# Optimization experiments

Hardware: AMD Instinct MI355X
Metric: run time of the kernel (lower is better)

The kernel has to match this reference:

```python
import jax, jax.numpy as jnp
import jax.lax as lax
import numpy as np

G = 128    # number of asset groups (batch)
A = 100    # n_assets per group
WIN = 10   # window_size
FD = 16    # feature_dim
H = 128    # hidden_dim


def setup_inputs() -> dict:
    key = jax.random.key(0)
    ks = jax.random.split(key, 12)
    N = G * A
    def glorot(k, shape, fan_in):
        return (jax.random.normal(k, shape, jnp.float32) / np.sqrt(fan_in)).astype(jnp.float32)
    return {
        "x": jax.random.normal(ks[0], (N, WIN, FD), jnp.float32),
        "W1": glorot(ks[1], (WIN * FD, H), WIN * FD),
        "b1": jnp.zeros((H,), jnp.float32),
        "W2": glorot(ks[2], (H, H), H),
        "b2": jnp.zeros((H,), jnp.float32),
        "W3": glorot(ks[3], (H, H), H),
        "b3": jnp.zeros((H,), jnp.float32),
        "cw1": glorot(ks[4], (H, 1, 1, 3), 3),      # conv2d_1 weight [out,in,kh,kw]
        "cb1": jnp.zeros((H,), jnp.float32),
        "cw2": glorot(ks[5], (1, H, 1, 3), 3 * H),  # conv2d_2 weight
        "cb2": jnp.zeros((1,), jnp.float32),
    }


def _corrcoef(r):
    xc = r - r.mean(axis=1, keepdims=True)
    cov = xc @ xc.T                      # divisor cancels in correlation
    d = jnp.sqrt(jnp.diag(cov))
    return cov / (d[:, None] * d[None, :])


def _conv1x3(h, w, b):
    # h: [1,C,N,H]; kernel (1,3), padding (0,1) -> NCHW conv
    out = lax.conv_general_dilated(h, w, (1, 1), ((0, 0), (1, 1)),
                                   dimension_numbers=("NCHW", "OIHW", "NCHW"))
    return out + b[None, :, None, None]


def reference(x, W1, b1, W2, b2, W3, b3, cw1, cb1, cw2, cb2):
    # block-diagonal adjacency == independent per-group adjacencies
    returns = x[:, :, -1].reshape(G, A, WIN)
    corr = jax.vmap(_corrcoef)(returns)                  # [G,A,A]
    adj = 1.0 - jnp.abs(corr) + jnp.eye(A, dtype=x.dtype)
    dinv = 1.0 / jnp.sqrt(adj.sum(axis=-1))              # [G,A]
    norm_adj = dinv[:, :, None] * adj * dinv[:, None, :] # D^-1/2 A D^-1/2

    feats = x.reshape(G, A, WIN * FD)
    h = jax.nn.relu(jnp.einsum("gij,gjf->gif", norm_adj, feats) @ W1 + b1)
    h = jax.nn.relu(jnp.einsum("gij,gjh->gih", norm_adj, h) @ W2 + b2)
    h = jax.nn.relu(jnp.einsum("gij,gjh->gih", norm_adj, h) @ W3 + b3)

    h = h.reshape(1, 1, G * A, H)                        # [1,1,N,H]
    h = jax.nn.relu(_conv1x3(h, cw1, cb1))               # [1,H,N,H]
    out = _conv1x3(h, cw2, cb2)                          # [1,1,N,H]
    return out[0, 0]                                     # [N,H]
```

## Files before the change

kernel.cpp:

```cpp
#include <hip/hip_runtime.h>

#define G   128
#define A   100
#define WIN 10
#define FD  16
#define H   128
#define NROWS (G*A)
#define K1  (WIN*FD)

#define SST 136
#define YST 136
#define AST 40
#define H3ST 132

typedef __attribute__((ext_vector_type(8))) short short8;
typedef __attribute__((ext_vector_type(4))) short short4v;
typedef __attribute__((ext_vector_type(4))) float floatx4;
typedef __attribute__((ext_vector_type(2))) float pf2;

struct BfPair { short h, l; };

__device__ inline unsigned short f2bf(float f) {
    unsigned u = __float_as_uint(f);
    u += 0x7fff + ((u >> 16) & 1);
    return (unsigned short)(u >> 16);
}
__device__ inline float bf2f(unsigned short h) {
    return __uint_as_float(((unsigned)h) << 16);
}
__device__ inline BfPair split1(float v) {
    BfPair p;
    unsigned short hb = f2bf(v);
    p.h = (short)hb;
    p.l = (short)f2bf(v - bf2f(hb));
    return p;
}

__global__ __launch_bounds__(256) void k_prep(const float* __restrict__ W1,
                                              const float* __restrict__ W2,
                                              const float* __restrict__ W3,
                                              short* __restrict__ Wh,
                                              short* __restrict__ Wl) {
    const int b = blockIdx.x, t = threadIdx.x;
    int l, kc;
    const float* Wsrc;
    if (b < 10)      { l = 0; kc = b;      Wsrc = W1; }
    else if (b < 18) { l = 1; kc = b - 10; Wsrc = W2; }
    else             { l = 2; kc = b - 18; Wsrc = W3; }
    short* dh = Wh + l * 128 * 160;
    short* dl = Wl + l * 128 * 160;
    for (int e = t; e < 16 * 128; e += 256) {
        int k = kc * 16 + (e >> 7), n = e & 127;
        BfPair p = split1(Wsrc[(size_t)k * H + n]);
        dh[n * 160 + k] = p.h;
        dl[n * 160 + k] = p.l;
    }
}

__global__ __launch_bounds__(1024) void k_mega(
    const float* __restrict__ x,
    const short* __restrict__ Whg, const short* __restrict__ Wlg,
    const float* __restrict__ b1, const float* __restrict__ b2,
    const float* __restrict__ b3,
    const float* __restrict__ cw1, const float* __restrict__ cb1,
    const float* __restrict__ cw2, const float* __restrict__ cb2,
    float* __restrict__ out)
{
    __shared__ short Ybuf[2 * 128 * YST];
    __shared__ short Sbuf[2 * 112 * SST];
    __shared__ short Abuf[2 * 112 * AST];
    __shared__ float wp2[64][16];
    __shared__ float xcT[WIN][104];
    __shared__ float invn[A];
    __shared__ float dinv[A];

    short* Yh = Ybuf;            short* Yl = Ybuf + 128 * YST;
    short* Sh = Sbuf;            short* Sl = Sbuf + 112 * SST;
    short* Ah = Abuf;            short* Al = Abuf + 112 * AST;
    float* adjs = (float*)Ybuf;
    float* h3f  = (float*)Sbuf;

    const int g = blockIdx.x >> 1, half = blockIdx.x & 1;
    const int t = threadIdx.x;
    const int wvid = t >> 6, lane = t & 63;
    const int quad = lane >> 4, r16 = lane & 15;

    if (t < H) {
        int cp = t >> 1, par = t & 1;
        wp2[cp][0  + par] = cw1[3 * t];
        wp2[cp][2  + par] = cw1[3 * t + 1];
        wp2[cp][4  + par] = cw1[3 * t + 2];
        wp2[cp][6  + par] = cb1[t];
        wp2[cp][8  + par] = cw2[3 * t];
        wp2[cp][10 + par] = cw2[3 * t + 1];
        wp2[cp][12 + par] = cw2[3 * t + 2];
        wp2[cp][14 + par] = cb2[0];
    }
    for (int e = t; e < A * WIN; e += 1024) {
        int a = e / WIN, wv = e % WIN;
        xcT[wv][a] = x[((g * A + a) * WIN + wv) * FD + (FD - 1)];
    }
    __syncthreads();
    if (t < A) {
        float m = 0.f;
        #pragma unroll
        for (int wv = 0; wv < WIN; wv++) m += xcT[wv][t];
        m *= (1.0f / WIN);
        float ss = 0.f;
        #pragma unroll
        for (int wv = 0; wv < WIN; wv++) {
            float v = xcT[wv][t] - m;
            xcT[wv][t] = v;
            ss += v * v;
        }
        invn[t] = rsqrtf(ss);
    }
    __syncthreads();
    for (int e = t; e < 2500; e += 1024) {
        int ti = e / 50, tj = e % 50;
        int i0 = 2 * ti, j0v = 2 * tj;
        float d00 = 0.f, d01 = 0.f, d10 = 0.f, d11 = 0.f;
        #pragma unroll
        for (int wv = 0; wv < WIN; wv++) {
            float2 xi = *(const float2*)&xcT[wv][i0];
            float2 xj = *(const float2*)&xcT[wv][j0v];
            d00 = fmaf(xi.x, xj.x, d00); d01 = fmaf(xi.x, xj.y, d01);
            d10 = fmaf(xi.y, xj.x, d10); d11 = fmaf(xi.y, xj.y, d11);
        }
        float ii0 = invn[i0], ii1 = invn[i0 + 1];
        float ij0 = invn[j0v], ij1 = invn[j0v + 1];
        float e2 = (ti == tj) ? 1.f : 0.f;
        adjs[i0 * 101 + j0v]           = 1.f - fabsf(d00 * ii0 * ij0) + e2;
        adjs[i0 * 101 + j0v + 1]       = 1.f - fabsf(d01 * ii0 * ij1);
        adjs[(i0 + 1) * 101 + j0v]     = 1.f - fabsf(d10 * ii1 * ij0);
        adjs[(i0 + 1) * 101 + j0v + 1] = 1.f - fabsf(d11 * ii1 * ij1) + e2;
    }
    __syncthreads();
    if (t < A) {
        float s = 0.f;
        for (int j = 0; j < A; j++) s += adjs[t * 101 + j];
        dinv[t] = rsqrtf(s);
    }
    __syncthreads();
    for (int e = t; e < 112 * 64; e += 1024) {
        int m = e >> 6, k2 = (e & 63) * 2;
        float v0 = (m < A && k2 < A)     ? dinv[m] * adjs[m * 101 + k2]     * dinv[k2]     : 0.f;
        float v1 = (m < A && k2 + 1 < A) ? dinv[m] * adjs[m * 101 + k2 + 1] * dinv[k2 + 1] : 0.f;
        BfPair p0 = split1(v0), p1 = split1(v1);
        *(short2*)&Sh[m * SST + k2] = make_short2(p0.h, p1.h);
        *(short2*)&Sl[m * SST + k2] = make_short2(p0.l, p1.l);
    }
    if (t < 384) {
        int r = 100 + (t >> 5), c = t & 31;
        Ah[r * AST + c] = 0; Al[r * AST + c] = 0;
    }
    __syncthreads();
    for (int e = t; e < 2048; e += 1024) {
        int n = e >> 4, k = 112 + (e & 15);
        Yh[n * YST + k] = 0; Yl[n * YST + k] = 0;
    }

    const int ntA  = wvid & 7;
    const int mtlo = (wvid < 8) ? 0 : 4;
    const int mcnt = (wvid < 8) ? 4 : 3;
    const int mtB  = wvid >> 1;
    const int ntB0 = (wvid & 1) * 4;

    for (int layer = 0; layer < 3; layer++) {
        const float* bg = (layer == 0) ? b1 : (layer == 1) ? b2 : b3;
        const short* wh = Whg + layer * 128 * 160;
        const short* wl = Wlg + layer * 128 * 160;
        const int nch = (layer == 0) ? 5 : 4;

        floatx4 acc[4];
        #pragma unroll
        for (int i = 0; i < 4; i++) acc[i] = (floatx4)0.f;

        for (int c = 0; c < nch; c++) {
            const int k0 = c << 5;
            size_t wo = (size_t)(ntA * 16 + r16) * 160 + k0 + quad * 8;
            short8 bh = *(const short8*)(wh + wo);
            short8 bl = *(const short8*)(wl + wo);
            if (layer == 0) {
                __syncthreads();
                if (t < 800) {
                    int r = t >> 3, q = t & 7;
                    float4 f = *(const float4*)(x + (size_t)(g * A + r) * K1 + k0 + q * 4);
                    float v[4] = {f.x, f.y, f.z, f.w};
                    short4v hh, ll;
                    #pragma unroll
                    for (int i = 0; i < 4; i++) {
                        BfPair p = split1(v[i]);
                        hh[i] = p.h; ll[i] = p.l;
                    }
                    *(short4v*)&Ah[r * AST + q * 4] = hh;
                    *(short4v*)&Al[r * AST + q * 4] = ll;
                }
                __syncthreads();
                for (int mi = 0; mi < mcnt; mi++) {
                    int mt = mtlo + mi;
                    short8 ah = *(const short8*)&Ah[(mt * 16 + r16) * AST + quad * 8];
                    short8 al = *(const short8*)&Al[(mt * 16 + r16) * AST + quad * 8];
                    acc[mi] = __builtin_amdgcn_mfma_f32_16x16x32_bf16(ah, bh, acc[mi], 0, 0, 0);
                    acc[mi] = __builtin_amdgcn_mfma_f32_16x16x32_bf16(ah, bl, acc[mi], 0, 0, 0);
                    acc[mi] = __builtin_amdgcn_mfma_f32_16x16x32_bf16(al, bh, acc[mi], 0, 0, 0);
                }
            } else {
                for (int mi = 0; mi < mcnt; mi++) {
                    int mt = mtlo + mi;
                    short8 ah = *(const short8*)&Yh[(mt * 16 + r16) * YST + k0 + quad * 8];
                    short8 al = *(const short8*)&Yl[(mt * 16 + r16) * YST + k0 + quad * 8];
                    acc[mi] = __builtin_amdgcn_mfma_f32_16x16x32_bf16(ah, bh, acc[mi], 0, 0, 0);
                    acc[mi] = __builtin_amdgcn_mfma_f32_16x16x32_bf16(ah, bl, acc[mi], 0, 0, 0);
                    acc[mi] = __builtin_amdgcn_mfma_f32_16x16x32_bf16(al, bh, acc[mi], 0, 0, 0);
                }
            }
        }
        __syncthreads();

        for (int mi = 0; mi < mcnt; mi++) {
            int mt = mtlo + mi;
            short4v yh4, yl4;
            #pragma unroll
            for (int rr = 0; rr < 4; rr++) {
                BfPair p = split1(acc[mi][rr]);
                yh4[rr] = p.h; yl4[rr] = p.l;
            }
            int off = (ntA * 16 + r16) * YST + mt * 16 + quad * 4;
            *(short4v*)&Yh[off] = yh4;
            *(short4v*)&Yl[off] = yl4;
        }
        __syncthreads();

        floatx4 accB[4];
        #pragma unroll
        for (int i = 0; i < 4; i++) accB[i] = (floatx4)0.f;
        if (mtB < 7) {
            #pragma unroll
            for (int c = 0; c < 4; c++) {
                const int k0 = c << 5;
                short8 ah = *(const short8*)&Sh[(mtB * 16 + r16) * SST + k0 + quad * 8];
                short8 al = *(const short8*)&Sl[(mtB * 16 + r16) * SST + k0 + quad * 8];
                #pragma unroll
                for (int j = 0; j < 4; j++) {
                    int nt = ntB0 + j;
                    short8 yh8 = *(const short8*)&Yh[(nt * 16 + r16) * YST + k0 + quad * 8];
                    short8 yl8 = *(const short8*)&Yl[(nt * 16 + r16) * YST + k0 + quad * 8];
                    accB[j] = __builtin_amdgcn_mfma_f32_16x16x32_bf16(ah, yh8, accB[j], 0, 0, 0);
                    accB[j] = __builtin_amdgcn_mfma_f32_16x16x32_bf16(ah, yl8, accB[j], 0, 0, 0);
                    accB[j] = __builtin_amdgcn_mfma_f32_16x16x32_bf16(al, yh8, accB[j], 0, 0, 0);
                }
            }
        }
        __syncthreads();

        if (mtB < 7) {
            #pragma unroll
            for (int j = 0; j < 4; j++) {
                int n = (ntB0 + j) * 16 + r16;
                float bv = bg[n];
                #pragma unroll
                for (int rr = 0; rr < 4; rr++) {
                    int m = mtB * 16 + quad * 4 + rr;
                    float v = fmaxf(0.f, accB[j][rr] + bv);
                    if (layer < 2) {
                        BfPair p = split1(v);
                        Yh[m * YST + n] = p.h;
                        Yl[m * YST + n] = p.l;
                    } else if (m < A) {
                        h3f[m * H3ST + n] = v;
                    }
                }
            }
        }
        __syncthreads();
    }

    if (t < 800) {
        const int row = t >> 4, q = t & 15;
        const int j0 = q * 8;
        const int r = half * 50 + row;
        const float* hr = h3f + (size_t)r * H3ST;

        float hh[12];
        if (q == 0) {
            hh[0] = 0.f; hh[1] = 0.f;
            #pragma unroll
            for (int i = 0; i < 10; i++) hh[2 + i] = hr[i];
        } else if (q == 15) {
            #pragma unroll
            for (int i = 0; i < 10; i++) hh[i] = hr[118 + i];
            hh[10] = 0.f; hh[11] = 0.f;
        } else {
            #pragma unroll
            for (int i = 0; i < 12; i++) hh[i] = hr[j0 - 2 + i];
        }
        const pf2 mlo2 = (pf2)((q == 0)  ? 0.f : 1.f);
        const pf2 mhi2 = (pf2)((q == 15) ? 0.f : 1.f);
        const pf2 zero2 = (pf2)0.f;

        pf2 accp[8];
        #pragma unroll
        for (int p = 0; p < 8; p++) accp[p] = zero2;

        #pragma unroll 2
        for (int cp = 0; cp < 64; cp++) {
            pf2 w0 = *(const pf2*)&wp2[cp][0];
            pf2 w1 = *(const pf2*)&wp2[cp][2];
            pf2 w2 = *(const pf2*)&wp2[cp][4];
            pf2 bb = *(const pf2*)&wp2[cp][6];
            pf2 v0 = *(const pf2*)&wp2[cp][8];
            pf2 v1 = *(const pf2*)&wp2[cp][10];
            pf2 v2 = *(const pf2*)&wp2[cp][12];
            pf2 tt[10];
            #pragma unroll
            for (int m = 0; m < 10; m++) {
                pf2 s = __builtin_elementwise_fma(w2, (pf2)hh[m + 2],
                        __builtin_elementwise_fma(w1, (pf2)hh[m + 1],
                        __builtin_elementwise_fma(w0, (pf2)hh[m], bb)));
                tt[m] = __builtin_elementwise_max(s, zero2);
            }
            tt[0] *= mlo2;
            tt[9] *= mhi2;
            #pragma unroll
            for (int p = 0; p < 8; p++)
                accp[p] = __builtin_elementwise_fma(v0, tt[p],
                          __builtin_elementwise_fma(v1, tt[p + 1],
                          __builtin_elementwise_fma(v2, tt[p + 2], accp[p])));
        }
        const float c2b = wp2[0][14];
        float o[8];
        #pragma unroll
        for (int p = 0; p < 8; p++) o[p] = accp[p].x + accp[p].y + c2b;
        float* op = out + ((size_t)g * A + r) * H + j0;
        *(float4*)op       = make_float4(o[0], o[1], o[2], o[3]);
        *(float4*)(op + 4) = make_float4(o[4], o[5], o[6], o[7]);
    }
}

extern "C" void kernel_launch(void* const* d_in, const int* in_sizes, int n_in,
                              void* d_out, int out_size, void* d_ws, size_t ws_size,
                              hipStream_t stream) {
    const float* x   = (const float*)d_in[0];
    const float* W1  = (const float*)d_in[1];
    const float* b1  = (const float*)d_in[2];
    const float* W2  = (const float*)d_in[3];
    const float* b2  = (const float*)d_in[4];
    const float* W3  = (const float*)d_in[5];
    const float* b3  = (const float*)d_in[6];
    const float* cw1 = (const float*)d_in[7];
    const float* cb1 = (const float*)d_in[8];
    const float* cw2 = (const float*)d_in[9];
    const float* cb2 = (const float*)d_in[10];
    float* out = (float*)d_out;

    short* Wh = (short*)d_ws;
    short* Wl = Wh + 3 * 128 * 160;

    k_prep<<<26, 256, 0, stream>>>(W1, W2, W3, Wh, Wl);
    k_mega<<<G * 2, 1024, 0, stream>>>(x, Wh, Wl, b1, b2, b3,
                                       cw1, cb1, cw2, cb2, out);
}
```

Measured before the change: 162.5 us.

## Load layer-0 input fragments directly from global into MFMA registers, drop LDS staging

Layer 0 no longer stages x chunks through a shared-memory A buffer with two barriers per K-chunk. Each lane now reads its 8 input floats straight from global memory, splits them into bf16 hi/lo in registers and feeds them to the MFMAs. Weight fragments for all K-chunks are preloaded into registers before the loop. The prep kernel is also restructured to one block per output column, so its transposed writes are contiguous. The trade-offs are more register pressure and uncoalesced, repeated global reads of x across waves that share rows, in exchange for fewer syncs and less LDS.

```diff
diff --git a/kernel.cpp b/kernel.cpp
--- a/kernel.cpp
+++ b/kernel.cpp
@@ -10,7 +10,6 @@
 
 #define SST 136
 #define YST 136
-#define AST 40
 #define H3ST 132
 
 typedef __attribute__((ext_vector_type(8))) short short8;
@@ -36,24 +35,21 @@
     return p;
 }
 
-__global__ __launch_bounds__(256) void k_prep(const float* __restrict__ W1,
-                                              const float* __restrict__ W2,
-                                              const float* __restrict__ W3,
-                                              short* __restrict__ Wh,
-                                              short* __restrict__ Wl) {
+__global__ __launch_bounds__(64) void k_prep(const float* __restrict__ W1,
+                                             const float* __restrict__ W2,
+                                             const float* __restrict__ W3,
+                                             short* __restrict__ Wh,
+                                             short* __restrict__ Wl) {
     const int b = blockIdx.x, t = threadIdx.x;
-    int l, kc;
-    const float* Wsrc;
-    if (b < 10)      { l = 0; kc = b;      Wsrc = W1; }
-    else if (b < 18) { l = 1; kc = b - 10; Wsrc = W2; }
-    else             { l = 2; kc = b - 18; Wsrc = W3; }
-    short* dh = Wh + l * 128 * 160;
-    short* dl = Wl + l * 128 * 160;
-    for (int e = t; e < 16 * 128; e += 256) {
-        int k = kc * 16 + (e >> 7), n = e & 127;
+    const int l = b >> 7, n = b & 127;
+    const int K = (l == 0) ? K1 : H;
+    const float* Wsrc = (l == 0) ? W1 : (l == 1) ? W2 : W3;
+    short* dh = Wh + l * 128 * 160 + n * 160;
+    short* dl = Wl + l * 128 * 160 + n * 160;
+    for (int k = t; k < K; k += 64) {
         BfPair p = split1(Wsrc[(size_t)k * H + n]);
-        dh[n * 160 + k] = p.h;
-        dl[n * 160 + k] = p.l;
+        dh[k] = p.h;
+        dl[k] = p.l;
     }
 }
 
@@ -68,7 +64,6 @@
 {
     __shared__ short Ybuf[2 * 128 * YST];
     __shared__ short Sbuf[2 * 112 * SST];
-    __shared__ short Abuf[2 * 112 * AST];
     __shared__ float wp2[64][16];
     __shared__ float xcT[WIN][104];
     __shared__ float invn[A];
@@ -76,7 +71,6 @@
 
     short* Yh = Ybuf;            short* Yl = Ybuf + 128 * YST;
     short* Sh = Sbuf;            short* Sl = Sbuf + 112 * SST;
-    short* Ah = Abuf;            short* Al = Abuf + 112 * AST;
     float* adjs = (float*)Ybuf;
     float* h3f  = (float*)Sbuf;
 
@@ -150,10 +144,6 @@
         *(short2*)&Sh[m * SST + k2] = make_short2(p0.h, p1.h);
         *(short2*)&Sl[m * SST + k2] = make_short2(p0.l, p1.l);
     }
-    if (t < 384) {
-        int r = 100 + (t >> 5), c = t & 31;
-        Ah[r * AST + c] = 0; Al[r * AST + c] = 0;
-    }
     __syncthreads();
     for (int e = t; e < 2048; e += 1024) {
         int n = e >> 4, k = 112 + (e & 15);
@@ -165,6 +155,7 @@
     const int mcnt = (wvid < 8) ? 4 : 3;
     const int mtB  = wvid >> 1;
     const int ntB0 = (wvid & 1) * 4;
+    const short8 z8 = (short8)0;
 
     for (int layer = 0; layer < 3; layer++) {
         const float* bg = (layer == 0) ? b1 : (layer == 1) ? b2 : b3;
@@ -172,51 +163,53 @@
         const short* wl = Wlg + layer * 128 * 160;
         const int nch = (layer == 0) ? 5 : 4;
 
+        short8 bhx[5], blx[5];
+        for (int c = 0; c < nch; c++) {
+            size_t wo = (size_t)(ntA * 16 + r16) * 160 + (c << 5) + quad * 8;
+            bhx[c] = *(const short8*)(wh + wo);
+            blx[c] = *(const short8*)(wl + wo);
+        }
+
         floatx4 acc[4];
         #pragma unroll
         for (int i = 0; i < 4; i++) acc[i] = (floatx4)0.f;
 
-        for (int c = 0; c < nch; c++) {
-            const int k0 = c << 5;
-            size_t wo = (size_t)(ntA * 16 + r16) * 160 + k0 + quad * 8;
-            short8 bh = *(const short8*)(wh + wo);
-            short8 bl = *(const short8*)(wl + wo);
-            if (layer == 0) {
-                __syncthreads();
-                if (t < 800) {
-                    int r = t >> 3, q = t & 7;
-                    float4 f = *(const float4*)(x + (size_t)(g * A + r) * K1 + k0 + q * 4);
-                    float v[4] = {f.x, f.y, f.z, f.w};
-                    short4v hh, ll;
-                    #pragma unroll
-                    for (int i = 0; i < 4; i++) {
-                        BfPair p = split1(v[i]);
-                        hh[i] = p.h; ll[i] = p.l;
-                    }
-                    *(short4v*)&Ah[r * AST + q * 4] = hh;
-                    *(short4v*)&Al[r * AST + q * 4] = ll;
+        if (layer == 0) {
+            for (int c = 0; c < 5; c++) {
+                const int k0 = c << 5;
+                for (int mi = 0; mi < mcnt; mi++) {
+                    int rm = (mtlo + mi) * 16 + r16;
+                    short8 ah, al;
+                    if (rm < A) {
+                        const float* gp = x + (size_t)(g * A + rm) * K1 + k0 + quad * 8;
+                        float4 f0 = *(const float4*)gp;
+                        float4 f1 = *(const float4*)(gp + 4);
+                        float v[8] = {f0.x, f0.y, f0.z, f0.w, f1.x, f1.y, f1.z, f1.w};
+                        #pragma unroll
+                        for (int i = 0; i < 8; i++) {
+                            BfPair p = split1(v[i]);
+                            ah[i] = p.h; al[i] = p.l;
+                        }
+                    } else { ah = z8; al = z8; }
+                    acc[mi] = __builtin_amdgcn_mfma_f32_16x16x32_bf16(ah, bhx[c], acc[mi], 0, 0, 0);
+                    acc[mi] = __builtin_amdgcn_mfma_f32_16x16x32_bf16(ah, blx[c], acc[mi], 0, 0, 0);
+                    acc[mi] = __builtin_amdgcn_mfma_f32_16x16x32_bf16(al, bhx[c], acc[mi], 0, 0, 0);
                 }
-                __syncthreads();
-                for (int mi = 0; mi < mcnt; mi++) {
-                    int mt = mtlo + mi;
-                    short8 ah = *(const short8*)&Ah[(mt * 16 + r16) * AST + quad * 8];
-                    short8 al = *(const short8*)&Al[(mt * 16 + r16) * AST + quad * 8];
-                    acc[mi] = __builtin_amdgcn_mfma_f32_16x16x32_bf16(ah, bh, acc[mi], 0, 0, 0);
-                    acc[mi] = __builtin_amdgcn_mfma_f32_16x16x32_bf16(ah, bl, acc[mi], 0, 0, 0);
-                    acc[mi] = __builtin_amdgcn_mfma_f32_16x16x32_bf16(al, bh, acc[mi], 0, 0, 0);
-                }
-            } else {
+            }
+        } else {
+            for (int c = 0; c < 4; c++) {
+                const int k0 = c << 5;
                 for (int mi = 0; mi < mcnt; mi++) {
                     int mt = mtlo + mi;
                     short8 ah = *(const short8*)&Yh[(mt * 16 + r16) * YST + k0 + quad * 8];
                     short8 al = *(const short8*)&Yl[(mt * 16 + r16) * YST + k0 + quad * 8];
-                    acc[mi] = __builtin_amdgcn_mfma_f32_16x16x32_bf16(ah, bh, acc[mi], 0, 0, 0);
-                    acc[mi] = __builtin_amdgcn_mfma_f32_16x16x32_bf16(ah, bl, acc[mi], 0, 0, 0);
-                    acc[mi] = __builtin_amdgcn_mfma_f32_16x16x32_bf16(al, bh, acc[mi], 0, 0, 0);
+                    acc[mi] = __builtin_amdgcn_mfma_f32_16x16x32_bf16(ah, bhx[c], acc[mi], 0, 0, 0);
+                    acc[mi] = __builtin_amdgcn_mfma_f32_16x16x32_bf16(ah, blx[c], acc[mi], 0, 0, 0);
+                    acc[mi] = __builtin_amdgcn_mfma_f32_16x16x32_bf16(al, bhx[c], acc[mi], 0, 0, 0);
                 }
             }
-        }
-        __syncthreads();
+            __syncthreads();
+        }
 
         for (int mi = 0; mi < mcnt; mi++) {
             int mt = mtlo + mi;
@@ -357,7 +350,7 @@
     short* Wh = (short*)d_ws;
     short* Wl = Wh + 3 * 128 * 160;
 
-    k_prep<<<26, 256, 0, stream>>>(W1, W2, W3, Wh, Wl);
+    k_prep<<<384, 64, 0, stream>>>(W1, W2, W3, Wh, Wl);
     k_mega<<<G * 2, 1024, 0, stream>>>(x, Wh, Wl, b1, b2, b3,
                                        cw1, cb1, cw2, cb2, out);
 }
```

After: 274.5 us. 68.9% more time.
